# Optimization experiments

Hardware: AMD Instinct MI355X
Metric: run time of the kernel (lower is better)

## Reference

```python
import jax, jax.numpy as jnp
import numpy as np

B, N, C = 8192, 4, 1024
H = 16
D = C // H              # head_dim = 64
P = 4                   # proj_dim (Linformer reduced length)
IDX_I, IDX_J = 1, 2     # Return_attn_way(use_cls=True, attn_selet_way=0)
SCALE = D ** -0.5


def setup_inputs() -> dict:
    key = jax.random.key(0)
    ks = jax.random.split(key, 6)
    std = 0.02
    x = jax.random.normal(ks[0], (B, N, C), dtype=jnp.float32)
    W_qkv = jax.random.normal(ks[1], (C, 3 * C), dtype=jnp.float32) * std   # qkv_bias=False
    W_proj = jax.random.normal(ks[2], (C, C), dtype=jnp.float32) * std
    b_proj = jnp.zeros((C,), dtype=jnp.float32)
    W_E = jax.random.normal(ks[3], (P, N), dtype=jnp.float32) * std         # torch Linear weight [out,in]
    W_F = jax.random.normal(ks[4], (P, N), dtype=jnp.float32) * std
    return {"x": x, "W_qkv": W_qkv, "W_proj": W_proj, "b_proj": b_proj,
            "W_E": W_E, "W_F": W_F}


def reference(x, W_qkv, W_proj, b_proj, W_E, W_F):
    b, n, c = x.shape
    # qkv projection -> [B,N,3,H,D] -> q,k,v each [B,H,N,D]
    qkv = (x @ W_qkv).reshape(b, n, 3, H, D)
    qkv = jnp.transpose(qkv, (2, 0, 3, 1, 4))
    q, k, v = qkv[0], qkv[1], qkv[2]
    q = q * SCALE  # q_norm/k_norm are Identity (qk_norm=False)

    # gathered single-token score: q[:,:,IDX_I,:] @ k[:,:,IDX_J,:].T -> [B,H,H]
    # (torch transpose(-2,-1) on the [B,H,D] slice swaps H and D)
    attn_sel = jnp.einsum('bhd,bgd->bhg', q[:, :, IDX_I, :], k[:, :, IDX_J, :])
    attn_sel_sig = jax.nn.sigmoid(attn_sel)

    # Linformer E/F projection along the sequence axis: [B,H,N,D] -> [B,H,P,D]
    k_low = jnp.einsum('bhnd,pn->bhpd', k, W_E)
    v_low = jnp.einsum('bhnd,pn->bhpd', v, W_F)

    # reduced softmax attention: [B,H,N,P]
    attn = jnp.einsum('bhnd,bhpd->bhnp', q, k_low)
    attn = jax.nn.softmax(attn, axis=-1)  # attn_drop is identity (p=0, eval)
    out = jnp.einsum('bhnp,bhpd->bhnd', attn, v_low)

    # merge heads and output projection
    out = jnp.transpose(out, (0, 2, 1, 3)).reshape(b, n, c)
    out = out @ W_proj.T + b_proj  # proj_drop identity
    return (out, attn_sel_sig)
```

## Files before the change

kernel.cpp:

```cpp
#include <hip/hip_runtime.h>
#include <hip/hip_bf16.h>

#define B_   8192
#define C_   1024
#define H_   16
#define M_   (B_ * 4)
#define K_   1024
#define N1_  3072

typedef __attribute__((ext_vector_type(8))) short short8;
typedef __attribute__((ext_vector_type(4))) float f32x4;
typedef __attribute__((ext_vector_type(8))) int   int8v;

__device__ __forceinline__ unsigned short f2bf(float f) {
  union { float f; unsigned u; } v; v.f = f;
  unsigned r = v.u + 0x7fffu + ((v.u >> 16) & 1u);
  return (unsigned short)(r >> 16);
}
__device__ __forceinline__ float bf2f(unsigned short u) {
  union { unsigned u; float f; } v; v.u = ((unsigned)u) << 16;
  return v.f;
}
__device__ __forceinline__ int pk_fp8(float a, float b, float c, float d) {
  int r = __builtin_amdgcn_cvt_pk_fp8_f32(a, b, 0, false);
  r = __builtin_amdgcn_cvt_pk_fp8_f32(c, d, r, true);
  return r;
}

__global__ __launch_bounds__(256) void cast_x_k(const float* __restrict__ x,
                                                unsigned char* __restrict__ x8,
                                                unsigned short* __restrict__ xsel) {
  const int row = blockIdx.x;
  const int tid = threadIdx.x;
  float4 v = ((const float4*)(x + (size_t)row * 1024))[tid];
  ((int*)(x8 + (size_t)row * 1024))[tid] = pk_fp8(v.x, v.y, v.z, v.w);
  const int n = row & 3;
  if (n == 1 || n == 2) {
    ushort4 o;
    o.x = f2bf(v.x); o.y = f2bf(v.y); o.z = f2bf(v.z); o.w = f2bf(v.w);
    ((ushort4*)(xsel + ((size_t)(n - 1) * 8192 + (row >> 2)) * 1024))[tid] = o;
  }
}

__global__ __launch_bounds__(256) void transpose_wqkv_k(const float* __restrict__ in,
                                                        unsigned short* __restrict__ outb,
                                                        unsigned char* __restrict__ out8) {
  __shared__ float t[32][33];
  int tx = threadIdx.x, ty = threadIdx.y;
  int j0 = blockIdx.x * 32, c0 = blockIdx.y * 32;
#pragma unroll
  for (int i = 0; i < 4; ++i)
    t[ty + i * 8][tx] = in[(size_t)(c0 + ty + i * 8) * N1_ + j0 + tx];
  __syncthreads();
#pragma unroll
  for (int i = 0; i < 4; ++i) {
    int j = j0 + ty + i * 8;
    float v = t[tx][ty + i * 8];
    if (j < 1024) v *= 0.125f;
    outb[(size_t)j * K_ + c0 + tx] = f2bf(v);
    out8[(size_t)j * K_ + c0 + tx] =
        (unsigned char)(__builtin_amdgcn_cvt_pk_fp8_f32(v * 32.f, v * 32.f, 0, false) & 0xff);
  }
}

__global__ __launch_bounds__(256) void cast_wproj_k(const float* __restrict__ in,
                                                    unsigned char* __restrict__ out) {
  int i = blockIdx.x * 256 + threadIdx.x;
  float4 v = ((const float4*)in)[i];
  ((int*)out)[i] = pk_fp8(v.x * 32.f, v.y * 32.f, v.z * 32.f, v.w * 32.f);
}

__global__ __launch_bounds__(256) void gemm_fixup(const unsigned short* __restrict__ A,
                                                  const unsigned short* __restrict__ B0,
                                                  unsigned short* __restrict__ Cbf) {
  __shared__ unsigned short lsA[128 * 32];
  __shared__ unsigned short lsB[128 * 32];
  const int K = 1024, Ncols = 1024;
  const int tid = threadIdx.x;
  const int wave = tid >> 6, lane = tid & 63;
  const int wm = (wave >> 1) * 64, wn = (wave & 1) * 64;
  const long tile_m = (long)blockIdx.y * 128, tile_n = (long)blockIdx.x * 128;
  const unsigned short* Bm = B0 + (tile_m >= 8192 ? (size_t)1024 * 1024 : 0);

  f32x4 acc[4][4] = {};
  const int ci0 = (wave * 2 + 0) * 64 + lane;
  const int ci1 = (wave * 2 + 1) * 64 + lane;
  const int r0 = ci0 >> 2, kc0 = (ci0 & 3) * 8;
  const int r1 = ci1 >> 2, kc1 = (ci1 & 3) * 8;
  const unsigned short* gA0 = A + (tile_m + r0) * K + kc0;
  const unsigned short* gA1 = A + (tile_m + r1) * K + kc1;
  const unsigned short* gB0 = Bm + (tile_n + r0) * K + kc0;
  const unsigned short* gB1 = Bm + (tile_n + r1) * K + kc1;
  unsigned short* dA0 = lsA + (wave * 2 + 0) * 512;
  unsigned short* dA1 = lsA + (wave * 2 + 1) * 512;
  unsigned short* dB0 = lsB + (wave * 2 + 0) * 512;
  unsigned short* dB1 = lsB + (wave * 2 + 1) * 512;
  const int r16 = lane & 15, q8 = (lane >> 4) * 8;

  for (int kt = 0; kt < K; kt += 32) {
    __builtin_amdgcn_global_load_lds((const __attribute__((address_space(1))) void*)(gA0 + kt),
                                     (__attribute__((address_space(3))) void*)dA0, 16, 0, 0);
    __builtin_amdgcn_global_load_lds((const __attribute__((address_space(1))) void*)(gA1 + kt),
                                     (__attribute__((address_space(3))) void*)dA1, 16, 0, 0);
    __builtin_amdgcn_global_load_lds((const __attribute__((address_space(1))) void*)(gB0 + kt),
                                     (__attribute__((address_space(3))) void*)dB0, 16, 0, 0);
    __builtin_amdgcn_global_load_lds((const __attribute__((address_space(1))) void*)(gB1 + kt),
                                     (__attribute__((address_space(3))) void*)dB1, 16, 0, 0);
    __syncthreads();
    short8 afr[4], bfr[4];
#pragma unroll
    for (int mi = 0; mi < 4; ++mi)
      afr[mi] = *(const short8*)&lsA[(wm + mi * 16 + r16) * 32 + q8];
#pragma unroll
    for (int ni = 0; ni < 4; ++ni)
      bfr[ni] = *(const short8*)&lsB[(wn + ni * 16 + r16) * 32 + q8];
#pragma unroll
    for (int mi = 0; mi < 4; ++mi)
#pragma unroll
      for (int ni = 0; ni < 4; ++ni)
        acc[mi][ni] = __builtin_amdgcn_mfma_f32_16x16x32_bf16(afr[mi], bfr[ni], acc[mi][ni], 0, 0, 0);
    __syncthreads();
  }
  const int cl = lane & 15, rq = (lane >> 4) * 4;
#pragma unroll
  for (int mi = 0; mi < 4; ++mi)
#pragma unroll
    for (int ni = 0; ni < 4; ++ni) {
      long col = tile_n + wn + ni * 16 + cl;
#pragma unroll
      for (int r = 0; r < 4; ++r) {
        long row = tile_m + wm + mi * 16 + rq + r;
        Cbf[(size_t)row * Ncols + col] = f2bf(acc[mi][ni][r]);
      }
    }
}

template <int OUTMODE>
__global__ __launch_bounds__(512) void gemm_mx(const unsigned char* __restrict__ A,
                                               const unsigned char* __restrict__ Bm,
                                               unsigned short* __restrict__ Cbf,
                                               float* __restrict__ Cf,
                                               const float* __restrict__ bias,
                                               int K, int Ncols, int sA, int sB) {
  __shared__ unsigned char lds[131072];

  const int tid = threadIdx.x;
  const int wave = tid >> 6, lane = tid & 63;
  const int wm = (wave >> 2) * 128;
  const int wn = (wave & 3) * 64;
  const long tile_m = (long)blockIdx.y * 256, tile_n = (long)blockIdx.x * 256;

  f32x4 acc[8][4] = {};

  unsigned offA[4], offB[4];
#pragma unroll
  for (int j = 0; j < 4; ++j) {
    int ci = j * 512 + tid;
    int blk = ci >> 10, idb = ci & 1023;
    int qg = idb >> 8, id = idb & 255;
    int r2 = (id >> 3) & 1, r3 = (id >> 4) & 1;
    int rr0 = ((id >> 1) & 1) ^ r2, rr1 = ((id >> 2) & 1) ^ r3;
    int row = rr0 | (rr1 << 1) | (r2 << 2) | (r3 << 3) | ((id >> 5) << 4);
    int half = (id & 1) ^ rr0;
    offA[j] = (unsigned)((tile_m + blk * 128 + row) * K + qg * 32 + half * 16);
    offB[j] = (unsigned)((tile_n + blk * 128 + row) * K + qg * 32 + half * 16);
  }

  const int hl = lane & 15, qg = lane >> 4;
  const int swz = (hl & 12) << 3;
  const int laneFragBase = qg * 4096 + ((hl * 32) ^ swz) + ((hl & 1) << 4);
  const int Abase = (wm >> 7) * 16384 + laneFragBase;
  const int Bbase = (wn >> 7) * 16384 + (wn & 64) * 32 + laneFragBase;

  auto stage_pair = [&](int kt, unsigned char* dA, unsigned char* dB, int j) {
    __builtin_amdgcn_global_load_lds(
        (const __attribute__((address_space(1))) void*)(A + offA[j] + kt),
        (__attribute__((address_space(3))) void*)(dA + j * 8192 + wave * 1024), 16, 0, 0);
    __builtin_amdgcn_global_load_lds(
        (const __attribute__((address_space(1))) void*)(Bm + offB[j] + kt),
        (__attribute__((address_space(3))) void*)(dB + j * 8192 + wave * 1024), 16, 0, 0);
  };

  const int NT = K >> 7;
  stage_pair(0, lds, lds + 32768, 0);
  stage_pair(0, lds, lds + 32768, 1);
  stage_pair(0, lds, lds + 32768, 2);
  stage_pair(0, lds, lds + 32768, 3);

  for (int t = 0; t < NT; ++t) {
    unsigned char* bA = lds + (t & 1) * 65536;
    unsigned char* bB = bA + 32768;
    unsigned char* nA = lds + ((t + 1) & 1) * 65536;
    unsigned char* nB = nA + 32768;
    const int ktn = (t + 1) << 7;

    if (t + 1 < NT) {
      stage_pair(ktn, nA, nB, 0);
      stage_pair(ktn, nA, nB, 1);
      asm volatile("s_waitcnt vmcnt(4)" ::: "memory");
    } else {
      asm volatile("s_waitcnt vmcnt(0)" ::: "memory");
    }
    __builtin_amdgcn_s_barrier();

    int8v bfr[4];
#pragma unroll
    for (int ni = 0; ni < 4; ++ni) {
      int ad = Bbase + ni * 512;
      int4 h0 = *(const int4*)(bB + ad);
      int4 h1 = *(const int4*)(bB + (ad ^ 16));
      bfr[ni] = int8v{h0.x, h0.y, h0.z, h0.w, h1.x, h1.y, h1.z, h1.w};
    }
    {
      int8v af[4];
#pragma unroll
      for (int mi = 0; mi < 4; ++mi) {
        int ad = Abase + mi * 512;
        int4 h0 = *(const int4*)(bA + ad);
        int4 h1 = *(const int4*)(bA + (ad ^ 16));
        af[mi] = int8v{h0.x, h0.y, h0.z, h0.w, h1.x, h1.y, h1.z, h1.w};
      }
      __builtin_amdgcn_s_setprio(1);
#pragma unroll
      for (int mi = 0; mi < 4; ++mi)
#pragma unroll
        for (int ni = 0; ni < 4; ++ni)
          acc[mi][ni] = __builtin_amdgcn_mfma_scale_f32_16x16x128_f8f6f4(
              af[mi], bfr[ni], acc[mi][ni], 0, 0, 0, sA, 0, sB);
      __builtin_amdgcn_s_setprio(0);
    }

    if (t + 1 < NT) {
      stage_pair(ktn, nA, nB, 2);
      stage_pair(ktn, nA, nB, 3);
    }
    {
      int8v af[4];
#pragma unroll
      for (int mi = 0; mi < 4; ++mi) {
        int ad = Abase + (mi + 4) * 512;
        int4 h0 = *(const int4*)(bA + ad);
        int4 h1 = *(const int4*)(bA + (ad ^ 16));
        af[mi] = int8v{h0.x, h0.y, h0.z, h0.w, h1.x, h1.y, h1.z, h1.w};
      }
      __builtin_amdgcn_s_setprio(1);
#pragma unroll
      for (int mi = 0; mi < 4; ++mi)
#pragma unroll
        for (int ni = 0; ni < 4; ++ni)
          acc[mi + 4][ni] = __builtin_amdgcn_mfma_scale_f32_16x16x128_f8f6f4(
              af[mi], bfr[ni], acc[mi + 4][ni], 0, 0, 0, sA, 0, sB);
      __builtin_amdgcn_s_setprio(0);
    }
    __builtin_amdgcn_s_barrier();
  }

  const int cl = lane & 15, rq = (lane >> 4) * 4;
#pragma unroll
  for (int mi = 0; mi < 8; ++mi)
#pragma unroll
    for (int ni = 0; ni < 4; ++ni) {
      long col = tile_n + wn + ni * 16 + cl;
      float bv = (OUTMODE == 1) ? bias[col] : 0.f;
#pragma unroll
      for (int r = 0; r < 4; ++r) {
        long row = tile_m + wm + mi * 16 + rq + r;
        if (OUTMODE == 0)
          Cbf[(size_t)row * Ncols + col] = f2bf(acc[mi][ni][r]);
        else
          Cf[(size_t)row * Ncols + col] = acc[mi][ni][r] + bv;
      }
    }
}

__global__ __launch_bounds__(256) void attn_mfma_k(const unsigned short* __restrict__ qkv,
                                                   const unsigned short* __restrict__ q1,
                                                   const unsigned short* __restrict__ k2,
                                                   const float* __restrict__ WE,
                                                   const float* __restrict__ WF,
                                                   unsigned char* __restrict__ hmid8,
                                                   float* __restrict__ attn_sel) {
  __shared__ float As[4][16 * 17 + 2];
  const int tid = threadIdx.x;
  const int wave = tid >> 6, lane = tid & 63;
  const int b = blockIdx.x * 4 + wave;
  const size_t qb = (size_t)b * 4 * N1_;
  const int hl = lane & 15, qg = lane >> 4;

  f32x4 accS[4][4] = {};
  f32x4 accSel = {};
#pragma unroll
  for (int ch = 0; ch < 2; ++ch) {
    const int off = ch * 32 + qg * 8;
    short8 qf[4], kf[4];
#pragma unroll
    for (int n = 0; n < 4; ++n)
      qf[n] = *(const short8*)(qkv + qb + (size_t)n * N1_ + 0 + hl * 64 + off);
#pragma unroll
    for (int m = 0; m < 4; ++m)
      kf[m] = *(const short8*)(qkv + qb + (size_t)m * N1_ + 1024 + hl * 64 + off);
#pragma unroll
    for (int n = 0; n < 4; ++n)
#pragma unroll
      for (int m = 0; m < 4; ++m)
        accS[n][m] = __builtin_amdgcn_mfma_f32_16x16x32_bf16(qf[n], kf[m], accS[n][m], 0, 0, 0);
    short8 qs = *(const short8*)(q1 + (size_t)b * 1024 + hl * 64 + off);
    short8 ks = *(const short8*)(k2 + (size_t)b * 1024 + hl * 64 + off);
    accSel = __builtin_amdgcn_mfma_f32_16x16x32_bf16(qs, ks, accSel, 0, 0, 0);
  }

#pragma unroll
  for (int r = 0; r < 4; ++r)
    attn_sel[(size_t)b * 256 + (qg * 4 + r) * 16 + hl] = 1.f / (1.f + __expf(-accSel[r]));

  if ((hl >> 2) == qg) {
    const int h = hl, rr = h & 3;
    float Sm[4][4];
#pragma unroll
    for (int n = 0; n < 4; ++n)
#pragma unroll
      for (int m = 0; m < 4; ++m) Sm[n][m] = accS[n][m][rr];
#pragma unroll
    for (int n = 0; n < 4; ++n) {
      float lg[4];
#pragma unroll
      for (int p = 0; p < 4; ++p)
        lg[p] = Sm[n][0] * WE[p * 4] + Sm[n][1] * WE[p * 4 + 1] +
                Sm[n][2] * WE[p * 4 + 2] + Sm[n][3] * WE[p * 4 + 3];
      float mx = fmaxf(fmaxf(lg[0], lg[1]), fmaxf(lg[2], lg[3]));
      float e0 = __expf(lg[0] - mx), e1 = __expf(lg[1] - mx);
      float e2 = __expf(lg[2] - mx), e3 = __expf(lg[3] - mx);
      float inv = 1.f / (e0 + e1 + e2 + e3);
      e0 *= inv; e1 *= inv; e2 *= inv; e3 *= inv;
#pragma unroll
      for (int m = 0; m < 4; ++m)
        As[wave][h * 17 + n * 4 + m] =
            e0 * WF[0 * 4 + m] + e1 * WF[1 * 4 + m] + e2 * WF[2 * 4 + m] + e3 * WF[3 * 4 + m];
    }
  }
  __syncthreads();

  {
    const int h = lane & 15, dg = lane >> 4;
    float Ap[4][4];
#pragma unroll
    for (int n = 0; n < 4; ++n)
#pragma unroll
      for (int m = 0; m < 4; ++m) Ap[n][m] = As[wave][h * 17 + n * 4 + m];

    float outv[4][16] = {};
#pragma unroll
    for (int m = 0; m < 4; ++m) {
      const unsigned short* vp = qkv + qb + (size_t)m * N1_ + 2048 + h * 64 + dg * 16;
      short8 v0 = *(const short8*)(vp);
      short8 v1 = *(const short8*)(vp + 8);
      float vf[16];
#pragma unroll
      for (int j = 0; j < 8; ++j) {
        vf[j] = bf2f((unsigned short)v0[j]);
        vf[8 + j] = bf2f((unsigned short)v1[j]);
      }
#pragma unroll
      for (int n = 0; n < 4; ++n)
#pragma unroll
        for (int d = 0; d < 16; ++d) outv[n][d] += Ap[n][m] * vf[d];
    }
#pragma unroll
    for (int n = 0; n < 4; ++n) {
      int w0 = pk_fp8(outv[n][0] * 32.f, outv[n][1] * 32.f, outv[n][2] * 32.f, outv[n][3] * 32.f);
      int w1 = pk_fp8(outv[n][4] * 32.f, outv[n][5] * 32.f, outv[n][6] * 32.f, outv[n][7] * 32.f);
      int w2 = pk_fp8(outv[n][8] * 32.f, outv[n][9] * 32.f, outv[n][10] * 32.f, outv[n][11] * 32.f);
      int w3 = pk_fp8(outv[n][12] * 32.f, outv[n][13] * 32.f, outv[n][14] * 32.f, outv[n][15] * 32.f);
      *(int4*)(hmid8 + ((size_t)b * 4 + n) * 1024 + h * 64 + dg * 16) = make_int4(w0, w1, w2, w3);
    }
  }
}

extern "C" void kernel_launch(void* const* d_in, const int* in_sizes, int n_in,
                              void* d_out, int out_size, void* d_ws, size_t ws_size,
                              hipStream_t stream) {
  (void)in_sizes; (void)n_in; (void)out_size; (void)ws_size;
  const float* x      = (const float*)d_in[0];
  const float* W_qkv  = (const float*)d_in[1];
  const float* W_proj = (const float*)d_in[2];
  const float* b_proj = (const float*)d_in[3];
  const float* W_E    = (const float*)d_in[4];
  const float* W_F    = (const float*)d_in[5];

  float* out0 = (float*)d_out;
  float* out1 = out0 + (size_t)M_ * C_;

  char* ws = (char*)d_ws;
  unsigned short* xsel   = (unsigned short*)(ws);
  unsigned short* wqkvTb = (unsigned short*)(ws + 33554432);
  unsigned short* qkv_bf = (unsigned short*)(ws);
  unsigned char*  x8     = (unsigned char*)(ws + 201326592);
  unsigned char*  hmid8  = x8;
  unsigned char*  wqkvT8 = (unsigned char*)(ws + 234881024);
  unsigned char*  wproj8 = (unsigned char*)(ws + 238026752);
  unsigned short* q1k2   = (unsigned short*)(ws + 239075328);

  cast_x_k<<<32768, 256, 0, stream>>>(x, x8, xsel);
  transpose_wqkv_k<<<dim3(96, 32), dim3(32, 8), 0, stream>>>(W_qkv, wqkvTb, wqkvT8);
  cast_wproj_k<<<1024, 256, 0, stream>>>(W_proj, wproj8);

  gemm_fixup<<<dim3(8, 128), 256, 0, stream>>>(xsel, wqkvTb, q1k2);

  gemm_mx<0><<<dim3(12, 128), 512, 0, stream>>>(x8, wqkvT8, qkv_bf, nullptr, nullptr,
                                                1024, 3072, 127, 122);

  attn_mfma_k<<<B_ / 4, 256, 0, stream>>>(qkv_bf, q1k2, q1k2 + (size_t)8192 * 1024,
                                          W_E, W_F, hmid8, out1);

  gemm_mx<1><<<dim3(4, 128), 512, 0, stream>>>(hmid8, wproj8, nullptr, out0, b_proj,
                                               1024, 1024, 122, 122);
}
```

Baseline: 556.6 us.

## Prepack FP8 weights into fragment order and load B directly to registers

The FP8 weight casts now write W_qkv and W_proj in a blocked layout that matches the MFMA B-fragment order. The GEMM reads B straight from global memory into registers instead of staging it through LDS, which halves LDS use and drops one barrier per k-step. Only A is still double-buffered through LDS. The cost is direct global-load latency on B without LDS reuse, and a full vmcnt(0) wait each iteration that reduces overlap. A single barrier per iteration may also risk a race when the A buffer is overwritten.

```diff
diff --git a/kernel.cpp b/kernel.cpp
--- a/kernel.cpp
+++ b/kernel.cpp
@@ -25,6 +25,12 @@
   int r = __builtin_amdgcn_cvt_pk_fp8_f32(a, b, 0, false);
   r = __builtin_amdgcn_cvt_pk_fp8_f32(c, d, r, true);
   return r;
+}
+
+__device__ __forceinline__ size_t bpack(int j, int c) {
+  return (size_t)(j >> 4) * 16384 + (size_t)(c >> 7) * 2048 +
+         (size_t)((c >> 4) & 1) * 1024 + (size_t)((c >> 5) & 3) * 256 +
+         (size_t)(j & 15) * 16 + (size_t)(c & 15);
 }
 
 __global__ __launch_bounds__(256) void cast_x_k(const float* __restrict__ x,
@@ -55,10 +61,11 @@
 #pragma unroll
   for (int i = 0; i < 4; ++i) {
     int j = j0 + ty + i * 8;
+    int c = c0 + tx;
     float v = t[tx][ty + i * 8];
     if (j < 1024) v *= 0.125f;
-    outb[(size_t)j * K_ + c0 + tx] = f2bf(v);
-    out8[(size_t)j * K_ + c0 + tx] =
+    outb[(size_t)j * K_ + c] = f2bf(v);
+    out8[bpack(j, c)] =
         (unsigned char)(__builtin_amdgcn_cvt_pk_fp8_f32(v * 32.f, v * 32.f, 0, false) & 0xff);
   }
 }
@@ -67,7 +74,9 @@
                                                     unsigned char* __restrict__ out) {
   int i = blockIdx.x * 256 + threadIdx.x;
   float4 v = ((const float4*)in)[i];
-  ((int*)out)[i] = pk_fp8(v.x * 32.f, v.y * 32.f, v.z * 32.f, v.w * 32.f);
+  int f = i * 4;
+  int j = f >> 10, c = f & 1023;
+  *(int*)(out + bpack(j, c)) = pk_fp8(v.x * 32.f, v.y * 32.f, v.z * 32.f, v.w * 32.f);
 }
 
 __global__ __launch_bounds__(256) void gemm_fixup(const unsigned short* __restrict__ A,
@@ -142,7 +151,7 @@
                                                float* __restrict__ Cf,
                                                const float* __restrict__ bias,
                                                int K, int Ncols, int sA, int sB) {
-  __shared__ unsigned char lds[131072];
+  __shared__ unsigned char lds[65536];
 
   const int tid = threadIdx.x;
   const int wave = tid >> 6, lane = tid & 63;
@@ -152,65 +161,56 @@
 
   f32x4 acc[8][4] = {};
 
-  unsigned offA[4], offB[4];
+  unsigned offA[4];
 #pragma unroll
   for (int j = 0; j < 4; ++j) {
     int ci = j * 512 + tid;
     int blk = ci >> 10, idb = ci & 1023;
-    int qg = idb >> 8, id = idb & 255;
+    int qgs = idb >> 8, id = idb & 255;
     int r2 = (id >> 3) & 1, r3 = (id >> 4) & 1;
     int rr0 = ((id >> 1) & 1) ^ r2, rr1 = ((id >> 2) & 1) ^ r3;
     int row = rr0 | (rr1 << 1) | (r2 << 2) | (r3 << 3) | ((id >> 5) << 4);
     int half = (id & 1) ^ rr0;
-    offA[j] = (unsigned)((tile_m + blk * 128 + row) * K + qg * 32 + half * 16);
-    offB[j] = (unsigned)((tile_n + blk * 128 + row) * K + qg * 32 + half * 16);
+    offA[j] = (unsigned)((tile_m + blk * 128 + row) * K + qgs * 32 + half * 16);
   }
 
   const int hl = lane & 15, qg = lane >> 4;
   const int swz = (hl & 12) << 3;
   const int laneFragBase = qg * 4096 + ((hl * 32) ^ swz) + ((hl & 1) << 4);
   const int Abase = (wm >> 7) * 16384 + laneFragBase;
-  const int Bbase = (wn >> 7) * 16384 + (wn & 64) * 32 + laneFragBase;
-
-  auto stage_pair = [&](int kt, unsigned char* dA, unsigned char* dB, int j) {
-    __builtin_amdgcn_global_load_lds(
-        (const __attribute__((address_space(1))) void*)(A + offA[j] + kt),
-        (__attribute__((address_space(3))) void*)(dA + j * 8192 + wave * 1024), 16, 0, 0);
-    __builtin_amdgcn_global_load_lds(
-        (const __attribute__((address_space(1))) void*)(Bm + offB[j] + kt),
-        (__attribute__((address_space(3))) void*)(dB + j * 8192 + wave * 1024), 16, 0, 0);
+
+  const unsigned char* gB = Bm + (size_t)((tile_n + wn) >> 4) * 16384 + (size_t)lane * 16;
+
+  auto stageA = [&](int kt, unsigned char* dA) {
+#pragma unroll
+    for (int j = 0; j < 4; ++j)
+      __builtin_amdgcn_global_load_lds(
+          (const __attribute__((address_space(1))) void*)(A + offA[j] + kt),
+          (__attribute__((address_space(3))) void*)(dA + j * 8192 + wave * 1024), 16, 0, 0);
   };
 
   const int NT = K >> 7;
-  stage_pair(0, lds, lds + 32768, 0);
-  stage_pair(0, lds, lds + 32768, 1);
-  stage_pair(0, lds, lds + 32768, 2);
-  stage_pair(0, lds, lds + 32768, 3);
+  stageA(0, lds);
 
   for (int t = 0; t < NT; ++t) {
-    unsigned char* bA = lds + (t & 1) * 65536;
-    unsigned char* bB = bA + 32768;
-    unsigned char* nA = lds + ((t + 1) & 1) * 65536;
-    unsigned char* nB = nA + 32768;
-    const int ktn = (t + 1) << 7;
-
-    if (t + 1 < NT) {
-      stage_pair(ktn, nA, nB, 0);
-      stage_pair(ktn, nA, nB, 1);
-      asm volatile("s_waitcnt vmcnt(4)" ::: "memory");
-    } else {
-      asm volatile("s_waitcnt vmcnt(0)" ::: "memory");
-    }
+    unsigned char* bA = lds + (t & 1) * 32768;
+
+    asm volatile("s_waitcnt vmcnt(0)" ::: "memory");
     __builtin_amdgcn_s_barrier();
 
+    const int kt16 = t * 2048;
     int8v bfr[4];
 #pragma unroll
     for (int ni = 0; ni < 4; ++ni) {
-      int ad = Bbase + ni * 512;
-      int4 h0 = *(const int4*)(bB + ad);
-      int4 h1 = *(const int4*)(bB + (ad ^ 16));
+      const unsigned char* bp = gB + (size_t)ni * 16384 + kt16;
+      int4 h0 = *(const int4*)bp;
+      int4 h1 = *(const int4*)(bp + 1024);
       bfr[ni] = int8v{h0.x, h0.y, h0.z, h0.w, h1.x, h1.y, h1.z, h1.w};
     }
+
+    if (t + 1 < NT)
+      stageA((t + 1) << 7, lds + ((t + 1) & 1) * 32768);
+
     {
       int8v af[4];
 #pragma unroll
@@ -229,11 +229,6 @@
               af[mi], bfr[ni], acc[mi][ni], 0, 0, 0, sA, 0, sB);
       __builtin_amdgcn_s_setprio(0);
     }
-
-    if (t + 1 < NT) {
-      stage_pair(ktn, nA, nB, 2);
-      stage_pair(ktn, nA, nB, 3);
-    }
     {
       int8v af[4];
 #pragma unroll
@@ -252,7 +247,6 @@
               af[mi], bfr[ni], acc[mi + 4][ni], 0, 0, 0, sA, 0, sB);
       __builtin_amdgcn_s_setprio(0);
     }
-    __builtin_amdgcn_s_barrier();
   }
 
   const int cl = lane & 15, rq = (lane >> 4) * 4;
```

Result: no change. 554.9 us (-0.3%).
